# Kernel tuning notes

Hardware: AMD Instinct MI355X
Metric: run time of the kernel (lower is better)

The kernel has to match this reference:

```python
import jax, jax.numpy as jnp
import numpy as np

D_MODEL = 1024
N_HEADS = 16
D_K = D_MODEL // N_HEADS
LN_EPS = 1e-5
NEG_INF = -1.0e9


def setup_inputs() -> dict:
    key = jax.random.key(0)
    ks = jax.random.split(key, 10)
    B, S, D = 8, 1024, D_MODEL
    scale = 1.0 / np.sqrt(D)
    return {
        "input_Q": jax.random.normal(ks[0], (B, S, D), jnp.float32),
        "input_K": jax.random.normal(ks[1], (B, S, D), jnp.float32),
        "input_V": jax.random.normal(ks[2], (B, S, D), jnp.float32),
        "attn_mask": jax.random.bernoulli(ks[3], 0.1, (B, S, S)),  # True = masked
        # torch Linear weights: [out_features, in_features]
        "W_Q": jax.random.normal(ks[4], (D, D), jnp.float32) * scale,
        "W_K": jax.random.normal(ks[5], (D, D), jnp.float32) * scale,
        "W_V": jax.random.normal(ks[6], (D, D), jnp.float32) * scale,
        "W_fc": jax.random.normal(ks[7], (D, D), jnp.float32) * scale,
        "ln_gamma": jnp.ones((D,), jnp.float32),
        "ln_beta": jnp.zeros((D,), jnp.float32),
    }


def _layer_norm(x, gamma, beta):
    mu = jnp.mean(x, axis=-1, keepdims=True)
    var = jnp.mean(jnp.square(x - mu), axis=-1, keepdims=True)
    return (x - mu) * jax.lax.rsqrt(var + LN_EPS) * gamma + beta


def reference(input_Q, input_K, input_V, attn_mask, W_Q, W_K, W_V, W_fc, ln_gamma, ln_beta):
    B, S, D = input_Q.shape
    # project and split heads: [B, H, S, d_k]
    def proj(x, W):
        return jnp.einsum('bsd,od->bso', x, W).reshape(B, -1, N_HEADS, D_K).transpose(0, 2, 1, 3)
    Q = proj(input_Q, W_Q)
    K = proj(input_K, W_K)
    V = proj(input_V, W_V)
    scores = jnp.einsum('bhqk,bhmk->bhqm', Q, K) / np.sqrt(D_K)  # [B,H,Sq,Sk]
    scores = jnp.where(attn_mask[:, None, :, :], NEG_INF, scores)
    attn = jax.nn.softmax(scores, axis=-1)
    context = jnp.einsum('bhqm,bhmd->bhqd', attn, V)
    context = context.transpose(0, 2, 1, 3).reshape(B, -1, N_HEADS * D_K)
    output = jnp.einsum('bsd,od->bso', context, W_fc)
    out = _layer_norm(output + input_Q, ln_gamma, ln_beta)
    return out, attn
```

## Files before the change

### kernel.cpp

```cpp
#include <hip/hip_runtime.h>

typedef __attribute__((ext_vector_type(8))) __bf16 bf16x8;
typedef __attribute__((ext_vector_type(4))) float f32x4;

#define SLEN 1024
#define DMODEL 1024
#define NHEADS 16
#define DKH 64
#define BATCH 8

__device__ __forceinline__ unsigned short f2bf(float f) {
  unsigned u = __builtin_bit_cast(unsigned, f);
  u += 0x7FFFu + ((u >> 16) & 1u);
  return (unsigned short)(u >> 16);
}

__device__ __forceinline__ void gload_lds16(const void* g, void* l) {
  __builtin_amdgcn_global_load_lds((const __attribute__((address_space(1))) unsigned int*)g,
                                   (__attribute__((address_space(3))) unsigned int*)l, 16, 0, 0);
}

__global__ void detect_mask(const unsigned char* __restrict__ m, int* __restrict__ flag) {
  int t = threadIdx.x;
  unsigned any = 0;
  for (int j = t; j < 4096; j += 64) any |= m[j * 4 + 1];
  unsigned long long b = __ballot(any != 0);
  if (t == 0) *flag = (b != 0) ? 1 : 0;
}

__global__ __launch_bounds__(256) void mask_pack(const unsigned char* __restrict__ m,
                                                 const int* __restrict__ flagp,
                                                 unsigned* __restrict__ mb) {
  long base = (long)blockIdx.x << 10;
  int tid = threadIdx.x;
  int flag = *flagp;
  unsigned nib;
  if (flag) {
    uchar4 v = ((const uchar4*)(m + base))[tid];
    nib = (v.x ? 1u : 0u) | (v.y ? 2u : 0u) | (v.z ? 4u : 0u) | (v.w ? 8u : 0u);
  } else {
    int4 v = ((const int4*)((const int*)m + base))[tid];
    nib = (v.x ? 1u : 0u) | (v.y ? 2u : 0u) | (v.z ? 4u : 0u) | (v.w ? 8u : 0u);
  }
  __shared__ unsigned char nibs[256];
  nibs[tid] = (unsigned char)nib;
  __syncthreads();
  if (tid < 32) {
    unsigned wv = 0;
#pragma unroll
    for (int i = 0; i < 8; i++) wv |= ((unsigned)nibs[tid * 8 + i]) << (i * 4);
    mb[((long)blockIdx.x << 5) + tid] = wv;
  }
}

__global__ __launch_bounds__(256) void cvt_all(
    const float* __restrict__ i0, const float* __restrict__ i1,
    const float* __restrict__ i2, const float* __restrict__ w0,
    const float* __restrict__ w1, const float* __restrict__ w2,
    const float* __restrict__ w3, unsigned short* __restrict__ xo0,
    unsigned short* __restrict__ xo1, unsigned short* __restrict__ xo2,
    unsigned short* __restrict__ wo0, unsigned short* __restrict__ wo1,
    unsigned short* __restrict__ wo2, unsigned short* __restrict__ wo3,
    int n8x, int n8w) {
  int which = blockIdx.y;
  const float* in;
  unsigned short* o;
  int n8;
  if (which < 3) {
    in = which == 0 ? i0 : which == 1 ? i1 : i2;
    o = which == 0 ? xo0 : which == 1 ? xo1 : xo2;
    n8 = n8x;
  } else {
    in = which == 3 ? w0 : which == 4 ? w1 : which == 5 ? w2 : w3;
    o = which == 3 ? wo0 : which == 4 ? wo1 : which == 5 ? wo2 : wo3;
    n8 = n8w;
  }
  int i = blockIdx.x * 256 + threadIdx.x;
  if (i >= n8) return;
  const float4* p = (const float4*)in;
  float4 f0 = p[2 * i], f1 = p[2 * i + 1];
  union { unsigned short us[8]; uint4 v; } pk;
  pk.us[0] = f2bf(f0.x); pk.us[1] = f2bf(f0.y); pk.us[2] = f2bf(f0.z); pk.us[3] = f2bf(f0.w);
  pk.us[4] = f2bf(f1.x); pk.us[5] = f2bf(f1.y); pk.us[6] = f2bf(f1.z); pk.us[7] = f2bf(f1.w);
  ((uint4*)o)[i] = pk.v;
}

__global__ __launch_bounds__(256) void gemm_proj3(
    const unsigned short* __restrict__ A0, const unsigned short* __restrict__ A1,
    const unsigned short* __restrict__ A2, const unsigned short* __restrict__ B0,
    const unsigned short* __restrict__ B1, const unsigned short* __restrict__ B2,
    unsigned short* __restrict__ O0, unsigned short* __restrict__ O1,
    unsigned short* __restrict__ O2) {
  const int z = blockIdx.z;
  const unsigned short* Ab = z == 0 ? A0 : z == 1 ? A1 : A2;
  const unsigned short* Bb = z == 0 ? B0 : z == 1 ? B1 : B2;
  unsigned short* obf = z == 0 ? O0 : z == 1 ? O1 : O2;
  const float scale = z == 0 ? 0.125f : 1.0f;

  const int m0 = blockIdx.x * 128;
  const int n0 = blockIdx.y * 128;
  const int tid = threadIdx.x;
  const int l = tid & 63;
  const int w = tid >> 6;
  const int wr = w >> 1, wc = w & 1;
  const int rl = l & 15, hi = l >> 4;

  __shared__ __attribute__((aligned(16))) unsigned short As[128 * 64];
  __shared__ __attribute__((aligned(16))) unsigned short Bs[128 * 64];

  f32x4 acc[4][4];
#pragma unroll
  for (int i = 0; i < 4; i++)
#pragma unroll
    for (int j = 0; j < 4; j++) acc[i][j] = f32x4{0.f, 0.f, 0.f, 0.f};

  for (int k0 = 0; k0 < 1024; k0 += 64) {
    __syncthreads();
#pragma unroll
    for (int i = 0; i < 4; i++) {
      int o = (i * 256 + tid) * 16;
      int row = o >> 7, cb = o & 127;
      int cbs = cb ^ ((row & 7) << 4);
      gload_lds16(Ab + (long)(m0 + row) * 1024 + k0 + (cbs >> 1), (char*)As + o);
    }
#pragma unroll
    for (int i = 0; i < 4; i++) {
      int o = (i * 256 + tid) * 16;
      int row = o >> 7, cb = o & 127;
      int cbs = cb ^ ((row & 7) << 4);
      gload_lds16(Bb + (long)(n0 + row) * 1024 + k0 + (cbs >> 1), (char*)Bs + o);
    }
    __syncthreads();

#pragma unroll
    for (int ks = 0; ks < 2; ks++) {
      int kb = ks * 64 + hi * 16;
      bf16x8 af[4], bfr[4];
#pragma unroll
      for (int mi = 0; mi < 4; mi++) {
        int row = wr * 64 + mi * 16 + rl;
        af[mi] = *(const bf16x8*)((const char*)As + row * 128 + (kb ^ ((row & 7) << 4)));
      }
#pragma unroll
      for (int ni = 0; ni < 4; ni++) {
        int row = wc * 64 + ni * 16 + rl;
        bfr[ni] = *(const bf16x8*)((const char*)Bs + row * 128 + (kb ^ ((row & 7) << 4)));
      }
#pragma unroll
      for (int mi = 0; mi < 4; mi++)
#pragma unroll
        for (int ni = 0; ni < 4; ni++)
          acc[mi][ni] = __builtin_amdgcn_mfma_f32_16x16x32_bf16(af[mi], bfr[ni], acc[mi][ni], 0, 0, 0);
    }
  }

  const int r0 = hi << 2;
#pragma unroll
  for (int mi = 0; mi < 4; mi++) {
#pragma unroll
    for (int ni = 0; ni < 4; ni++) {
      f32x4 v = acc[mi][ni];
      int row = m0 + wr * 64 + mi * 16 + r0;
      int col = n0 + wc * 64 + ni * 16 + rl;
      if (z == 2) {
        union { unsigned short us[4]; unsigned long long vv; } pk;
        pk.us[0] = f2bf(v[0]); pk.us[1] = f2bf(v[1]);
        pk.us[2] = f2bf(v[2]); pk.us[3] = f2bf(v[3]);
        long idx = ((long)(((row >> 10) * 16 + (col >> 6)) * 64 + (col & 63)) << 10) + (row & 1023);
        *(unsigned long long*)&obf[idx] = pk.vv;
      } else {
#pragma unroll
        for (int j = 0; j < 4; j++) {
          int rr = row + j;
          long idx = (((long)((rr >> 10) * 16 + (col >> 6)) * 1024 + (rr & 1023)) << 6) + (col & 63);
          obf[idx] = f2bf(v[j] * scale);
        }
      }
    }
  }
}

__global__ __launch_bounds__(256) void gemm_fc(
    const unsigned short* __restrict__ Ab, const unsigned short* __restrict__ Bb,
    float* __restrict__ of32) {
  const int m0 = blockIdx.x * 128;
  const int n0 = blockIdx.y * 128;
  const int tid = threadIdx.x;
  const int l = tid & 63;
  const int w = tid >> 6;
  const int wr = w >> 1, wc = w & 1;
  const int rl = l & 15, hi = l >> 4;

  __shared__ __attribute__((aligned(16))) unsigned short As[128 * 64];
  __shared__ __attribute__((aligned(16))) unsigned short Bs[128 * 64];

  f32x4 acc[4][4];
#pragma unroll
  for (int i = 0; i < 4; i++)
#pragma unroll
    for (int j = 0; j < 4; j++) acc[i][j] = f32x4{0.f, 0.f, 0.f, 0.f};

  for (int k0 = 0; k0 < 1024; k0 += 64) {
    __syncthreads();
#pragma unroll
    for (int i = 0; i < 4; i++) {
      int o = (i * 256 + tid) * 16;
      int row = o >> 7, cb = o & 127;
      int cbs = cb ^ ((row & 7) << 4);
      gload_lds16(Ab + (long)(m0 + row) * 1024 + k0 + (cbs >> 1), (char*)As + o);
    }
#pragma unroll
    for (int i = 0; i < 4; i++) {
      int o = (i * 256 + tid) * 16;
      int row = o >> 7, cb = o & 127;
      int cbs = cb ^ ((row & 7) << 4);
      gload_lds16(Bb + (long)(n0 + row) * 1024 + k0 + (cbs >> 1), (char*)Bs + o);
    }
    __syncthreads();

#pragma unroll
    for (int ks = 0; ks < 2; ks++) {
      int kb = ks * 64 + hi * 16;
      bf16x8 af[4], bfr[4];
#pragma unroll
      for (int mi = 0; mi < 4; mi++) {
        int row = wr * 64 + mi * 16 + rl;
        af[mi] = *(const bf16x8*)((const char*)As + row * 128 + (kb ^ ((row & 7) << 4)));
      }
#pragma unroll
      for (int ni = 0; ni < 4; ni++) {
        int row = wc * 64 + ni * 16 + rl;
        bfr[ni] = *(const bf16x8*)((const char*)Bs + row * 128 + (kb ^ ((row & 7) << 4)));
      }
#pragma unroll
      for (int mi = 0; mi < 4; mi++)
#pragma unroll
        for (int ni = 0; ni < 4; ni++)
          acc[mi][ni] = __builtin_amdgcn_mfma_f32_16x16x32_bf16(af[mi], bfr[ni], acc[mi][ni], 0, 0, 0);
    }
  }

  const int r0 = hi << 2;
#pragma unroll
  for (int mi = 0; mi < 4; mi++) {
#pragma unroll
    for (int ni = 0; ni < 4; ni++) {
      f32x4 v = acc[mi][ni];
      int row = m0 + wr * 64 + mi * 16 + r0;
      int col = n0 + wc * 64 + ni * 16 + rl;
#pragma unroll
      for (int j = 0; j < 4; j++)
        of32[((long)(row + j) << 10) + col] = v[j];
    }
  }
}

__global__ __launch_bounds__(256) void attn_fused2(
    const unsigned short* __restrict__ Qh, const unsigned short* __restrict__ Kh,
    const unsigned short* __restrict__ Vt, const unsigned* __restrict__ mb,
    float* __restrict__ attn, unsigned short* __restrict__ ctx) {
  const int lin = blockIdx.x;
  const int xcd = lin & 7;
  const int k_ = lin >> 3;
  const int z = xcd + ((k_ >> 3) << 3);
  const int qt = k_ & 7;
  const int b = z >> 4, h = z & 15;
  const int tid = threadIdx.x, l = tid & 63, w = tid >> 6;
  const int rl = l & 15, hi = l >> 4;

  __shared__ __attribute__((aligned(16))) unsigned short Pl[16 * 1024];
  __shared__ float redm[4][16], reds[4][16];

  const long bh = (long)z * (SLEN * DKH);
  const unsigned short* Kb = Kh + bh;
  const unsigned short* Vb = Vt + bh;
  const long abase = (long)z << 20;

  bf16x8 qf0, qf1;
  {
    const unsigned short* qp = Qh + bh + (long)(qt * 128 + rl) * 64 + hi * 8;
    qf0 = *(const bf16x8*)qp;
    qf1 = *(const bf16x8*)(qp + 32);
  }

  for (int s = 0; s < 8; s++) {
    const int q0 = qt * 128 + s * 16;

    f32x4 acc[16];
#pragma unroll
    for (int t = 0; t < 16; t++) acc[t] = f32x4{0.f, 0.f, 0.f, 0.f};

    __builtin_amdgcn_s_setprio(1);
#pragma unroll
    for (int t = 0; t < 16; t++) {
      int col = w * 256 + t * 16 + rl;
      const unsigned short* kp = Kb + (long)col * 64 + hi * 8;
      bf16x8 k0 = *(const bf16x8*)kp;
      bf16x8 k1 = *(const bf16x8*)(kp + 32);
      acc[t] = __builtin_amdgcn_mfma_f32_16x16x32_bf16(k0, qf0, acc[t], 0, 0, 0);
      acc[t] = __builtin_amdgcn_mfma_f32_16x16x32_bf16(k1, qf1, acc[t], 0, 0, 0);
    }
    __builtin_amdgcn_s_setprio(0);

    unsigned mw[8];
    {
      const uint4* wp = (const uint4*)(mb + (((long)((b << 10) | (q0 + rl))) << 5) + w * 8);
      uint4 w0 = wp[0], w1 = wp[1];
      mw[0] = w0.x; mw[1] = w0.y; mw[2] = w0.z; mw[3] = w0.w;
      mw[4] = w1.x; mw[5] = w1.y; mw[6] = w1.z; mw[7] = w1.w;
    }

    float mx = -3.0e38f;
#pragma unroll
    for (int t = 0; t < 16; t++) {
#pragma unroll
      for (int j = 0; j < 4; j++) {
        unsigned bit = (mw[t >> 1] >> (((t & 1) << 4) + (hi << 2) + j)) & 1u;
        float v = bit ? -1.0e9f : acc[t][j];
        acc[t][j] = v;
        mx = fmaxf(mx, v);
      }
    }
    mx = fmaxf(mx, __shfl_xor(mx, 16));
    mx = fmaxf(mx, __shfl_xor(mx, 32));
    float sum = 0.f;
#pragma unroll
    for (int t = 0; t < 16; t++)
#pragma unroll
      for (int j = 0; j < 4; j++) {
        float e = __expf(acc[t][j] - mx);
        acc[t][j] = e;
        sum += e;
      }
    sum += __shfl_xor(sum, 16);
    sum += __shfl_xor(sum, 32);
    if (hi == 0) { redm[w][rl] = mx; reds[w][rl] = sum; }
    __syncthreads();
    float M, S, inv;
    {
      float m0_ = redm[0][rl], m1_ = redm[1][rl], m2_ = redm[2][rl], m3_ = redm[3][rl];
      M = fmaxf(fmaxf(m0_, m1_), fmaxf(m2_, m3_));
      S = reds[0][rl] * __expf(m0_ - M) + reds[1][rl] * __expf(m1_ - M) +
          reds[2][rl] * __expf(m2_ - M) + reds[3][rl] * __expf(m3_ - M);
      inv = __expf(mx - M) / S;
    }

#pragma unroll
    for (int t = 0; t < 16; t++) {
      int c0 = w * 256 + t * 16 + hi * 4;
      union { unsigned short us[4]; unsigned long long v; } pk;
      pk.us[0] = f2bf(acc[t][0] * inv);
      pk.us[1] = f2bf(acc[t][1] * inv);
      pk.us[2] = f2bf(acc[t][2] * inv);
      pk.us[3] = f2bf(acc[t][3] * inv);
      *(unsigned long long*)((char*)Pl + rl * 2048 + ((c0 * 2) ^ ((rl & 7) << 4))) = pk.v;
    }
    __syncthreads();

    {
      const long arow = abase + ((long)q0 << 10) + tid * 4;
#pragma unroll
      for (int i = 0; i < 16; i++) {
        unsigned long long pv8 = *(const unsigned long long*)(
            (const char*)Pl + i * 2048 + ((tid * 8) ^ ((i & 7) << 4)));
        f32x4 o4;
        o4[0] = __builtin_bit_cast(float, (unsigned)((pv8 & 0xFFFFu) << 16));
        o4[1] = __builtin_bit_cast(float, (unsigned)(((pv8 >> 16) & 0xFFFFu) << 16));
        o4[2] = __builtin_bit_cast(float, (unsigned)(((pv8 >> 32) & 0xFFFFu) << 16));
        o4[3] = __builtin_bit_cast(float, (unsigned)(((pv8 >> 48) & 0xFFFFu) << 16));
        __builtin_nontemporal_store(o4, (f32x4*)&attn[arow + ((long)i << 10)]);
      }
    }

    if (s < 7) {
      const unsigned short* qp = Qh + bh + (long)(q0 + 16 + rl) * 64 + hi * 8;
      qf0 = *(const bf16x8*)qp;
      qf1 = *(const bf16x8*)(qp + 32);
    }

    f32x4 c2 = f32x4{0.f, 0.f, 0.f, 0.f};
    __builtin_amdgcn_s_setprio(1);
#pragma unroll
    for (int ks = 0; ks < 32; ks++) {
      bf16x8 af = *(const bf16x8*)((const char*)Pl + rl * 2048 + ((ks * 64 + hi * 16) ^ ((rl & 7) << 4)));
      bf16x8 vf = *(const bf16x8*)(Vb + (long)(w * 16 + rl) * 1024 + ks * 32 + hi * 8);
      c2 = __builtin_amdgcn_mfma_f32_16x16x32_bf16(af, vf, c2, 0, 0, 0);
    }
    __builtin_amdgcn_s_setprio(0);

#pragma unroll
    for (int j = 0; j < 4; j++) {
      __builtin_nontemporal_store(
          f2bf(c2[j]),
          &ctx[((long)(b * 1024 + q0 + hi * 4 + j) << 10) + h * 64 + w * 16 + rl]);
    }
  }
}

__global__ __launch_bounds__(256) void ln_kernel(const float* __restrict__ fc,
                                                 const float* __restrict__ inQ,
                                                 const float* __restrict__ gamma,
                                                 const float* __restrict__ beta,
                                                 float* __restrict__ out) {
  long base = (long)blockIdx.x << 10;
  int tid = threadIdx.x, l = tid & 63, w = tid >> 6;
  float4 a = ((const float4*)(fc + base))[tid];
  float4 b = ((const float4*)(inQ + base))[tid];
  float4 x; x.x = a.x + b.x; x.y = a.y + b.y; x.z = a.z + b.z; x.w = a.w + b.w;
  float s = x.x + x.y + x.z + x.w;
  float q = x.x * x.x + x.y * x.y + x.z * x.z + x.w * x.w;
  for (int o = 32; o; o >>= 1) { s += __shfl_xor(s, o); q += __shfl_xor(q, o); }
  __shared__ float rs[4], rq[4];
  if (l == 0) { rs[w] = s; rq[w] = q; }
  __syncthreads();
  s = rs[0] + rs[1] + rs[2] + rs[3];
  q = rq[0] + rq[1] + rq[2] + rq[3];
  float mu = s * (1.0f / 1024.0f);
  float var = q * (1.0f / 1024.0f) - mu * mu;
  float rstd = rsqrtf(var + 1e-5f);
  float4 g = ((const float4*)gamma)[tid];
  float4 be = ((const float4*)beta)[tid];
  float4 o4;
  o4.x = (x.x - mu) * rstd * g.x + be.x;
  o4.y = (x.y - mu) * rstd * g.y + be.y;
  o4.z = (x.z - mu) * rstd * g.z + be.z;
  o4.w = (x.w - mu) * rstd * g.w + be.w;
  ((float4*)(out + base))[tid] = o4;
}

extern "C" void kernel_launch(void* const* d_in, const int* in_sizes, int n_in,
                              void* d_out, int out_size, void* d_ws, size_t ws_size,
                              hipStream_t stream) {
  const float* inQ = (const float*)d_in[0];
  const float* inK = (const float*)d_in[1];
  const float* inV = (const float*)d_in[2];
  const unsigned char* mask = (const unsigned char*)d_in[3];
  const float* WQ = (const float*)d_in[4];
  const float* WK = (const float*)d_in[5];
  const float* WV = (const float*)d_in[6];
  const float* WFC = (const float*)d_in[7];
  const float* gamma = (const float*)d_in[8];
  const float* beta = (const float*)d_in[9];

  float* out = (float*)d_out;
  float* attn = out + (size_t)BATCH * SLEN * DMODEL;

  char* ws = (char*)d_ws;
  size_t off = 256;
  int* flag = (int*)ws;
  auto take = [&](size_t bytes) { char* p = ws + off; off += (bytes + 255) & ~255UL; return p; };
  const size_t XB = (size_t)BATCH * SLEN * DMODEL * 2;
  const size_t WB = (size_t)DMODEL * DMODEL * 2;
  unsigned short* Xq = (unsigned short*)take(XB);
  unsigned short* Xk = (unsigned short*)take(XB);
  unsigned short* Xv = (unsigned short*)take(XB);
  unsigned short* Wqb = (unsigned short*)take(WB);
  unsigned short* Wkb = (unsigned short*)take(WB);
  unsigned short* Wvb = (unsigned short*)take(WB);
  unsigned short* Wfcb = (unsigned short*)take(WB);
  unsigned short* Qh = (unsigned short*)take(XB);
  unsigned short* Kh = (unsigned short*)take(XB);
  unsigned short* Vt = (unsigned short*)take(XB);
  unsigned short* ctx = (unsigned short*)take(XB);
  float* fc = (float*)take((size_t)BATCH * SLEN * DMODEL * 4);
  unsigned* mb = (unsigned*)take((size_t)BATCH * SLEN * 32 * 4);

  detect_mask<<<1, 64, 0, stream>>>(mask, flag);
  mask_pack<<<BATCH * SLEN, 256, 0, stream>>>(mask, flag, mb);

  const int n8x = BATCH * SLEN * DMODEL / 8;
  const int n8w = DMODEL * DMODEL / 8;
  cvt_all<<<dim3(n8x / 256, 7), 256, 0, stream>>>(inQ, inK, inV, WQ, WK, WV, WFC,
                                                  Xq, Xk, Xv, Wqb, Wkb, Wvb, Wfcb,
                                                  n8x, n8w);

  gemm_proj3<<<dim3(64, 8, 3), 256, 0, stream>>>(Xq, Xk, Xv, Wqb, Wkb, Wvb, Qh, Kh, Vt);

  attn_fused2<<<dim3(1024), 256, 0, stream>>>(Qh, Kh, Vt, mb, attn, ctx);

  gemm_fc<<<dim3(64, 8), 256, 0, stream>>>(ctx, Wfcb, fc);

  ln_kernel<<<BATCH * SLEN, 256, 0, stream>>>(fc, inQ, gamma, beta, out);
}
```

Before: 343.7 us.

## Fuse fp32-to-bf16 input conversion into projection GEMM and remap blocks per XCD

Drops the separate conversion pass over the three 32MB fp32 activation tensors. The projection GEMM now reads fp32 inputs directly, converts them to bf16 in registers and stores them swizzled into LDS. The block index is also remapped so that consecutive M tiles land on the same XCD, aiming for better L2 reuse of the A rows. The cost is that each A tile is re-read as fp32 once per N tile (8 times), and the A loads become synchronous register loads instead of async global_load_lds.

```diff
diff --git a/kernel.cpp b/kernel.cpp
--- a/kernel.cpp
+++ b/kernel.cpp
@@ -53,28 +53,14 @@
   }
 }
 
-__global__ __launch_bounds__(256) void cvt_all(
-    const float* __restrict__ i0, const float* __restrict__ i1,
-    const float* __restrict__ i2, const float* __restrict__ w0,
-    const float* __restrict__ w1, const float* __restrict__ w2,
-    const float* __restrict__ w3, unsigned short* __restrict__ xo0,
-    unsigned short* __restrict__ xo1, unsigned short* __restrict__ xo2,
-    unsigned short* __restrict__ wo0, unsigned short* __restrict__ wo1,
-    unsigned short* __restrict__ wo2, unsigned short* __restrict__ wo3,
-    int n8x, int n8w) {
+__global__ __launch_bounds__(256) void cvt_w(
+    const float* __restrict__ w0, const float* __restrict__ w1,
+    const float* __restrict__ w2, const float* __restrict__ w3,
+    unsigned short* __restrict__ o0, unsigned short* __restrict__ o1,
+    unsigned short* __restrict__ o2, unsigned short* __restrict__ o3, int n8) {
   int which = blockIdx.y;
-  const float* in;
-  unsigned short* o;
-  int n8;
-  if (which < 3) {
-    in = which == 0 ? i0 : which == 1 ? i1 : i2;
-    o = which == 0 ? xo0 : which == 1 ? xo1 : xo2;
-    n8 = n8x;
-  } else {
-    in = which == 3 ? w0 : which == 4 ? w1 : which == 5 ? w2 : w3;
-    o = which == 3 ? wo0 : which == 4 ? wo1 : which == 5 ? wo2 : wo3;
-    n8 = n8w;
-  }
+  const float* in = which == 0 ? w0 : which == 1 ? w1 : which == 2 ? w2 : w3;
+  unsigned short* o = which == 0 ? o0 : which == 1 ? o1 : which == 2 ? o2 : o3;
   int i = blockIdx.x * 256 + threadIdx.x;
   if (i >= n8) return;
   const float4* p = (const float4*)in;
@@ -86,19 +72,22 @@
 }
 
 __global__ __launch_bounds__(256) void gemm_proj3(
-    const unsigned short* __restrict__ A0, const unsigned short* __restrict__ A1,
-    const unsigned short* __restrict__ A2, const unsigned short* __restrict__ B0,
+    const float* __restrict__ A0, const float* __restrict__ A1,
+    const float* __restrict__ A2, const unsigned short* __restrict__ B0,
     const unsigned short* __restrict__ B1, const unsigned short* __restrict__ B2,
     unsigned short* __restrict__ O0, unsigned short* __restrict__ O1,
     unsigned short* __restrict__ O2) {
-  const int z = blockIdx.z;
-  const unsigned short* Ab = z == 0 ? A0 : z == 1 ? A1 : A2;
+  const int z = blockIdx.y;
+  const float* Af = z == 0 ? A0 : z == 1 ? A1 : A2;
   const unsigned short* Bb = z == 0 ? B0 : z == 1 ? B1 : B2;
   unsigned short* obf = z == 0 ? O0 : z == 1 ? O1 : O2;
   const float scale = z == 0 ? 0.125f : 1.0f;
 
-  const int m0 = blockIdx.x * 128;
-  const int n0 = blockIdx.y * 128;
+  const int bid = blockIdx.x;
+  const int xcd = bid & 7;
+  const int local = bid >> 3;
+  const int m0 = (xcd * 8 + (local >> 3)) * 128;
+  const int n0 = (local & 7) * 128;
   const int tid = threadIdx.x;
   const int l = tid & 63;
   const int w = tid >> 6;
@@ -117,11 +106,22 @@
   for (int k0 = 0; k0 < 1024; k0 += 64) {
     __syncthreads();
 #pragma unroll
-    for (int i = 0; i < 4; i++) {
-      int o = (i * 256 + tid) * 16;
-      int row = o >> 7, cb = o & 127;
-      int cbs = cb ^ ((row & 7) << 4);
-      gload_lds16(Ab + (long)(m0 + row) * 1024 + k0 + (cbs >> 1), (char*)As + o);
+    for (int i = 0; i < 2; i++) {
+      int c = i * 256 + tid;
+      int row = c >> 2, kc = (c & 3) << 4;
+      const float* src = Af + (long)(m0 + row) * 1024 + k0 + kc;
+      float4 f0 = ((const float4*)src)[0];
+      float4 f1 = ((const float4*)src)[1];
+      float4 f2 = ((const float4*)src)[2];
+      float4 f3 = ((const float4*)src)[3];
+      union { unsigned short us[8]; uint4 v; } pa, pb;
+      pa.us[0] = f2bf(f0.x); pa.us[1] = f2bf(f0.y); pa.us[2] = f2bf(f0.z); pa.us[3] = f2bf(f0.w);
+      pa.us[4] = f2bf(f1.x); pa.us[5] = f2bf(f1.y); pa.us[6] = f2bf(f1.z); pa.us[7] = f2bf(f1.w);
+      pb.us[0] = f2bf(f2.x); pb.us[1] = f2bf(f2.y); pb.us[2] = f2bf(f2.z); pb.us[3] = f2bf(f2.w);
+      pb.us[4] = f2bf(f3.x); pb.us[5] = f2bf(f3.y); pb.us[6] = f2bf(f3.z); pb.us[7] = f2bf(f3.w);
+      int c0 = kc >> 3, sw = row & 7;
+      *(uint4*)((char*)As + row * 128 + ((c0 ^ sw) << 4)) = pa.v;
+      *(uint4*)((char*)As + row * 128 + (((c0 + 1) ^ sw) << 4)) = pb.v;
     }
 #pragma unroll
     for (int i = 0; i < 4; i++) {
@@ -451,9 +451,6 @@
   auto take = [&](size_t bytes) { char* p = ws + off; off += (bytes + 255) & ~255UL; return p; };
   const size_t XB = (size_t)BATCH * SLEN * DMODEL * 2;
   const size_t WB = (size_t)DMODEL * DMODEL * 2;
-  unsigned short* Xq = (unsigned short*)take(XB);
-  unsigned short* Xk = (unsigned short*)take(XB);
-  unsigned short* Xv = (unsigned short*)take(XB);
   unsigned short* Wqb = (unsigned short*)take(WB);
   unsigned short* Wkb = (unsigned short*)take(WB);
   unsigned short* Wvb = (unsigned short*)take(WB);
@@ -468,13 +465,11 @@
   detect_mask<<<1, 64, 0, stream>>>(mask, flag);
   mask_pack<<<BATCH * SLEN, 256, 0, stream>>>(mask, flag, mb);
 
-  const int n8x = BATCH * SLEN * DMODEL / 8;
   const int n8w = DMODEL * DMODEL / 8;
-  cvt_all<<<dim3(n8x / 256, 7), 256, 0, stream>>>(inQ, inK, inV, WQ, WK, WV, WFC,
-                                                  Xq, Xk, Xv, Wqb, Wkb, Wvb, Wfcb,
-                                                  n8x, n8w);
-
-  gemm_proj3<<<dim3(64, 8, 3), 256, 0, stream>>>(Xq, Xk, Xv, Wqb, Wkb, Wvb, Qh, Kh, Vt);
+  cvt_w<<<dim3(n8w / 256, 4), 256, 0, stream>>>(WQ, WK, WV, WFC,
+                                                Wqb, Wkb, Wvb, Wfcb, n8w);
+
+  gemm_proj3<<<dim3(512, 3), 256, 0, stream>>>(inQ, inK, inV, Wqb, Wkb, Wvb, Qh, Kh, Vt);
 
   attn_fused2<<<dim3(1024), 256, 0, stream>>>(Qh, Kh, Vt, mb, attn, ctx);
 
```

Measured after the change: 356.2 us. 1.04x slower.

## Double attention block to 512 threads with split-K PV reduction

Applied to the files above, without the earlier changes.

Runs the fused attention kernel with 8 waves instead of 4. Each wave now computes scores for 128 key columns instead of 256, and the attn store loop splits rows between two thread halves. The PV product is split along K across wave pairs and reduced through a small LDS buffer with an extra barrier. The aim is more waves per block to hide memory latency and lower per-thread register pressure, at the cost of an extra sync and more cross-wave reduction.

```diff
diff --git a/kernel.cpp b/kernel.cpp
--- a/kernel.cpp
+++ b/kernel.cpp
@@ -255,7 +255,7 @@
   }
 }
 
-__global__ __launch_bounds__(256) void attn_fused2(
+__global__ __launch_bounds__(512) void attn_fused2(
     const unsigned short* __restrict__ Qh, const unsigned short* __restrict__ Kh,
     const unsigned short* __restrict__ Vt, const unsigned* __restrict__ mb,
     float* __restrict__ attn, unsigned short* __restrict__ ctx) {
@@ -269,7 +269,8 @@
   const int rl = l & 15, hi = l >> 4;
 
   __shared__ __attribute__((aligned(16))) unsigned short Pl[16 * 1024];
-  __shared__ float redm[4][16], reds[4][16];
+  __shared__ float redm[8][16], reds[8][16];
+  __shared__ __attribute__((aligned(16))) float Pp[4][64][4];
 
   const long bh = (long)z * (SLEN * DKH);
   const unsigned short* Kb = Kh + bh;
@@ -286,14 +287,14 @@
   for (int s = 0; s < 8; s++) {
     const int q0 = qt * 128 + s * 16;
 
-    f32x4 acc[16];
-#pragma unroll
-    for (int t = 0; t < 16; t++) acc[t] = f32x4{0.f, 0.f, 0.f, 0.f};
+    f32x4 acc[8];
+#pragma unroll
+    for (int t = 0; t < 8; t++) acc[t] = f32x4{0.f, 0.f, 0.f, 0.f};
 
     __builtin_amdgcn_s_setprio(1);
 #pragma unroll
-    for (int t = 0; t < 16; t++) {
-      int col = w * 256 + t * 16 + rl;
+    for (int t = 0; t < 8; t++) {
+      int col = w * 128 + t * 16 + rl;
       const unsigned short* kp = Kb + (long)col * 64 + hi * 8;
       bf16x8 k0 = *(const bf16x8*)kp;
       bf16x8 k1 = *(const bf16x8*)(kp + 32);
@@ -302,17 +303,15 @@
     }
     __builtin_amdgcn_s_setprio(0);
 
-    unsigned mw[8];
+    unsigned mw[4];
     {
-      const uint4* wp = (const uint4*)(mb + (((long)((b << 10) | (q0 + rl))) << 5) + w * 8);
-      uint4 w0 = wp[0], w1 = wp[1];
+      uint4 w0 = *(const uint4*)(mb + (((long)((b << 10) | (q0 + rl))) << 5) + w * 4);
       mw[0] = w0.x; mw[1] = w0.y; mw[2] = w0.z; mw[3] = w0.w;
-      mw[4] = w1.x; mw[5] = w1.y; mw[6] = w1.z; mw[7] = w1.w;
     }
 
     float mx = -3.0e38f;
 #pragma unroll
-    for (int t = 0; t < 16; t++) {
+    for (int t = 0; t < 8; t++) {
 #pragma unroll
       for (int j = 0; j < 4; j++) {
         unsigned bit = (mw[t >> 1] >> (((t & 1) << 4) + (hi << 2) + j)) & 1u;
@@ -325,7 +324,7 @@
     mx = fmaxf(mx, __shfl_xor(mx, 32));
     float sum = 0.f;
 #pragma unroll
-    for (int t = 0; t < 16; t++)
+    for (int t = 0; t < 8; t++)
 #pragma unroll
       for (int j = 0; j < 4; j++) {
         float e = __expf(acc[t][j] - mx);
@@ -338,16 +337,18 @@
     __syncthreads();
     float M, S, inv;
     {
-      float m0_ = redm[0][rl], m1_ = redm[1][rl], m2_ = redm[2][rl], m3_ = redm[3][rl];
-      M = fmaxf(fmaxf(m0_, m1_), fmaxf(m2_, m3_));
-      S = reds[0][rl] * __expf(m0_ - M) + reds[1][rl] * __expf(m1_ - M) +
-          reds[2][rl] * __expf(m2_ - M) + reds[3][rl] * __expf(m3_ - M);
+      M = -3.0e38f;
+#pragma unroll
+      for (int ww = 0; ww < 8; ww++) M = fmaxf(M, redm[ww][rl]);
+      S = 0.f;
+#pragma unroll
+      for (int ww = 0; ww < 8; ww++) S += reds[ww][rl] * __expf(redm[ww][rl] - M);
       inv = __expf(mx - M) / S;
     }
 
 #pragma unroll
-    for (int t = 0; t < 16; t++) {
-      int c0 = w * 256 + t * 16 + hi * 4;
+    for (int t = 0; t < 8; t++) {
+      int c0 = w * 128 + t * 16 + hi * 4;
       union { unsigned short us[4]; unsigned long long v; } pk;
       pk.us[0] = f2bf(acc[t][0] * inv);
       pk.us[1] = f2bf(acc[t][1] * inv);
@@ -358,17 +359,20 @@
     __syncthreads();
 
     {
-      const long arow = abase + ((long)q0 << 10) + tid * 4;
-#pragma unroll
-      for (int i = 0; i < 16; i++) {
+      const int half = tid >> 8;
+      const int t8 = tid & 255;
+      const long arow = abase + ((long)q0 << 10) + t8 * 4;
+#pragma unroll
+      for (int i = 0; i < 8; i++) {
+        int row = i * 2 + half;
         unsigned long long pv8 = *(const unsigned long long*)(
-            (const char*)Pl + i * 2048 + ((tid * 8) ^ ((i & 7) << 4)));
+            (const char*)Pl + row * 2048 + ((t8 * 8) ^ ((row & 7) << 4)));
         f32x4 o4;
         o4[0] = __builtin_bit_cast(float, (unsigned)((pv8 & 0xFFFFu) << 16));
         o4[1] = __builtin_bit_cast(float, (unsigned)(((pv8 >> 16) & 0xFFFFu) << 16));
         o4[2] = __builtin_bit_cast(float, (unsigned)(((pv8 >> 32) & 0xFFFFu) << 16));
         o4[3] = __builtin_bit_cast(float, (unsigned)(((pv8 >> 48) & 0xFFFFu) << 16));
-        __builtin_nontemporal_store(o4, (f32x4*)&attn[arow + ((long)i << 10)]);
+        __builtin_nontemporal_store(o4, (f32x4*)&attn[arow + ((long)row << 10)]);
       }
     }
 
@@ -378,21 +382,30 @@
       qf1 = *(const bf16x8*)(qp + 32);
     }
 
+    const int d4 = w & 3, kh = w >> 2;
     f32x4 c2 = f32x4{0.f, 0.f, 0.f, 0.f};
     __builtin_amdgcn_s_setprio(1);
 #pragma unroll
-    for (int ks = 0; ks < 32; ks++) {
+    for (int k16 = 0; k16 < 16; k16++) {
+      int ks = kh * 16 + k16;
       bf16x8 af = *(const bf16x8*)((const char*)Pl + rl * 2048 + ((ks * 64 + hi * 16) ^ ((rl & 7) << 4)));
-      bf16x8 vf = *(const bf16x8*)(Vb + (long)(w * 16 + rl) * 1024 + ks * 32 + hi * 8);
+      bf16x8 vf = *(const bf16x8*)(Vb + (long)(d4 * 16 + rl) * 1024 + ks * 32 + hi * 8);
       c2 = __builtin_amdgcn_mfma_f32_16x16x32_bf16(af, vf, c2, 0, 0, 0);
     }
     __builtin_amdgcn_s_setprio(0);
 
-#pragma unroll
-    for (int j = 0; j < 4; j++) {
-      __builtin_nontemporal_store(
-          f2bf(c2[j]),
-          &ctx[((long)(b * 1024 + q0 + hi * 4 + j) << 10) + h * 64 + w * 16 + rl]);
+    if (w < 4) {
+      *(f32x4*)Pp[w][l] = c2;
+    }
+    __syncthreads();
+    if (w >= 4) {
+      f32x4 p = *(const f32x4*)Pp[w - 4][l];
+#pragma unroll
+      for (int j = 0; j < 4; j++) {
+        __builtin_nontemporal_store(
+            f2bf(c2[j] + p[j]),
+            &ctx[((long)(b * 1024 + q0 + hi * 4 + j) << 10) + h * 64 + d4 * 16 + rl]);
+      }
     }
   }
 }
@@ -476,7 +489,7 @@
 
   gemm_proj3<<<dim3(64, 8, 3), 256, 0, stream>>>(Xq, Xk, Xv, Wqb, Wkb, Wvb, Qh, Kh, Vt);
 
-  attn_fused2<<<dim3(1024), 256, 0, stream>>>(Qh, Kh, Vt, mb, attn, ctx);
+  attn_fused2<<<dim3(1024), 512, 0, stream>>>(Qh, Kh, Vt, mb, attn, ctx);
 
   gemm_fc<<<dim3(64, 8), 256, 0, stream>>>(ctx, Wfcb, fc);
 
```

Result: faster. 306.1 us (median of 2 runs) (-10.9%).
